# Performance work log

Hardware: AMD Instinct MI355X
Metric: run time of the kernel (lower is better)

Reference implementation:

```python
import jax, jax.numpy as jnp
import numpy as np

N = 4096          # samples per domain
D_IN = 512        # input feature dim
H = 10            # hidden size of featurizer
D_OUT = 50        # featurizer output dim


def setup_inputs() -> dict:
    key = jax.random.key(0)
    ks = jax.random.split(key, 12)
    def lin(k, fan_in, fan_out):
        bound = 1.0 / np.sqrt(fan_in)
        kw, kb = jax.random.split(k)
        W = jax.random.uniform(kw, (fan_in, fan_out), jnp.float32, -bound, bound)
        b = jax.random.uniform(kb, (fan_out,), jnp.float32, -bound, bound)
        return W, b
    W1, b1 = lin(ks[0], D_IN, H)
    W2, b2 = lin(ks[1], H, H)
    W3, b3 = lin(ks[2], H, H)
    W4, b4 = lin(ks[3], H, D_OUT)
    Xs = jax.random.normal(ks[4], (N, D_IN), jnp.float32)
    Xt = jax.random.normal(ks[5], (N, D_IN), jnp.float32) + 0.1
    # epsilonOPT = log(rand(1) * 1e-10)
    epsilonOPT = jnp.log(jax.random.uniform(ks[6], (1,), jnp.float32) * 1e-10)
    sigmaOPT = jnp.sqrt(jnp.asarray(2.0 * 32 * 32, jnp.float32))
    sigma0OPT = jnp.sqrt(jnp.asarray(0.005, jnp.float32))
    return {"Xs": Xs, "Xt": Xt, "W1": W1, "b1": b1, "W2": W2, "b2": b2,
            "W3": W3, "b3": b3, "W4": W4, "b4": b4,
            "epsilonOPT": epsilonOPT, "sigmaOPT": sigmaOPT, "sigma0OPT": sigma0OPT}


def _pdist2(x, y):
    # squared pairwise distances, clamped at 0 (as in Pdist2)
    xn = jnp.sum(x * x, axis=1)[:, None]
    yn = jnp.sum(y * y, axis=1)[None, :]
    d = xn + yn - 2.0 * (x @ y.T)
    return jnp.maximum(d, 0.0)


def _featurize(x, W1, b1, W2, b2, W3, b3, W4, b4):
    sp = jax.nn.softplus
    h = sp(x @ W1 + b1)
    h = sp(h @ W2 + b2)
    h = sp(h @ W3 + b3)
    return h @ W4 + b4


def _deep_kernel(Dd, Do, ep, sigma, sigma0):
    # (1-ep)*exp(-Dd/sigma0 - Do/sigma) + ep*exp(-Do/sigma)   (L=1)
    e_org = jnp.exp(-Do / sigma)
    return (1.0 - ep) * jnp.exp(-Dd / sigma0) * e_org + ep * e_org


def reference(Xs, Xt, W1, b1, W2, b2, W3, b3, W4, b4, epsilonOPT, sigmaOPT, sigma0OPT):
    n = Xs.shape[0]
    Fea_org = jnp.concatenate([Xs, Xt], axis=0)
    Fea = _featurize(Fea_org, W1, b1, W2, b2, W3, b3, W4, b4)

    ep = jax.nn.sigmoid(epsilonOPT)[0]
    sigma = sigmaOPT ** 2
    sigma0 = sigma0OPT ** 2

    X, Y = Fea[:n], Fea[n:]
    Xo, Yo = Fea_org[:n], Fea_org[n:]

    Kx = _deep_kernel(_pdist2(X, X), _pdist2(Xo, Xo), ep, sigma, sigma0)
    Ky = _deep_kernel(_pdist2(Y, Y), _pdist2(Yo, Yo), ep, sigma, sigma0)
    Kxy = _deep_kernel(_pdist2(X, Y), _pdist2(Xo, Yo), ep, sigma, sigma0)

    nx = n
    ny = Fea.shape[0] - n
    # unbiased estimator with use_1sample_U=True
    xx = (jnp.sum(Kx) - jnp.trace(Kx)) / (nx * (nx - 1))
    yy = (jnp.sum(Ky) - jnp.trace(Ky)) / (ny * (ny - 1))
    xy = (jnp.sum(Kxy) - jnp.trace(Kxy)) / (nx * (ny - 1))
    mmd2 = xx - 2.0 * xy + yy
    return mmd2
```

## Files before the change

### kernel.cpp

```cpp
#include <hip/hip_runtime.h>
#include <math.h>

#define NHALF 4096
#define NTOT  8192
#define DIN   512
#define DFR   50
#define FPS   160
#define BM    128
#define NBI   64
#define NTRI  2080
#define T64STRIDE 524288
#define KCSTRIDE  65536

typedef short short8 __attribute__((ext_vector_type(8)));
typedef float f32x4 __attribute__((ext_vector_type(4)));
typedef int   i32x8 __attribute__((ext_vector_type(8)));

__device__ __forceinline__ float softplus_f(float x) {
    return fmaxf(x, 0.f) + log1pf(expf(-fabsf(x)));
}

__device__ __forceinline__ unsigned cvt_pk_bf16(float lo, float hi) {
    unsigned r;
    asm("v_cvt_pk_bf16_f32 %0, %1, %2" : "=v"(r) : "v"(lo), "v"(hi));
    return r;
}

__device__ __forceinline__ unsigned short bf16_rne(float v) {
    return (unsigned short)(cvt_pk_bf16(v, 0.f) & 0xffffu);
}

__device__ __forceinline__ float bf16_to_f(unsigned short s) {
    union { unsigned u; float f; } c;
    c.u = (unsigned)s << 16;
    return c.f;
}

__device__ __forceinline__ void gload_lds16(const void* g, void* l) {
    __builtin_amdgcn_global_load_lds(
        (const __attribute__((address_space(1))) void*)g,
        (__attribute__((address_space(3))) void*)l, 16, 0, 0);
}

__global__ __launch_bounds__(256) void featurize_kernel(
    const float* __restrict__ Xs, const float* __restrict__ Xt,
    const float* __restrict__ W1, const float* __restrict__ b1,
    const float* __restrict__ W2, const float* __restrict__ b2,
    const float* __restrict__ W3, const float* __restrict__ b3,
    const float* __restrict__ W4, const float* __restrict__ b4,
    const float* __restrict__ sigP, const float* __restrict__ sig0P,
    unsigned short* __restrict__ FpkA, unsigned short* __restrict__ FpkB,
    float* __restrict__ normC, char* __restrict__ Xb8)
{
    __shared__ float W1L[80 * 65];
    __shared__ __align__(16) unsigned short pkA[4][FPS];
    __shared__ __align__(16) unsigned short pkB[4][FPS];
    int tid = threadIdx.x;
    for (int e = tid; e < 5120; e += 256) {
        int r = e / 10, j = e - 10 * r;
        W1L[((r & 7) * 10 + j) * 65 + (r >> 3)] = W1[e];
    }
    __syncthreads();

    int row  = (blockIdx.x * blockDim.x + tid) >> 6;
    int lane = tid & 63, wv = tid >> 6;
    float alpha8 = 64.f / sigP[0];
    float beta   = 64.f / sig0P[0];
    const float* src = (row < NHALF) ? (Xs + (size_t)row * DIN)
                                     : (Xt + (size_t)(row - NHALF) * DIN);
    float4 v0 = ((const float4*)src)[lane * 2];
    float4 v1 = ((const float4*)src)[lane * 2 + 1];
    float x[8] = {v0.x, v0.y, v0.z, v0.w, v1.x, v1.y, v1.z, v1.w};

    float z[8];
#pragma unroll
    for (int t = 0; t < 8; ++t) z[t] = x[t] * alpha8;
    unsigned w0 = 0, w1 = 0;
    w0 = __builtin_amdgcn_cvt_pk_fp8_f32(z[0], z[1], w0, false);
    w0 = __builtin_amdgcn_cvt_pk_fp8_f32(z[2], z[3], w0, true);
    w1 = __builtin_amdgcn_cvt_pk_fp8_f32(z[4], z[5], w1, false);
    w1 = __builtin_amdgcn_cvt_pk_fp8_f32(z[6], z[7], w1, true);
    float on = 0.f, qf;
    qf = __builtin_amdgcn_cvt_f32_fp8(w0, 0); on = fmaf(qf, qf, on);
    qf = __builtin_amdgcn_cvt_f32_fp8(w0, 1); on = fmaf(qf, qf, on);
    qf = __builtin_amdgcn_cvt_f32_fp8(w0, 2); on = fmaf(qf, qf, on);
    qf = __builtin_amdgcn_cvt_f32_fp8(w0, 3); on = fmaf(qf, qf, on);
    qf = __builtin_amdgcn_cvt_f32_fp8(w1, 0); on = fmaf(qf, qf, on);
    qf = __builtin_amdgcn_cvt_f32_fp8(w1, 1); on = fmaf(qf, qf, on);
    qf = __builtin_amdgcn_cvt_f32_fp8(w1, 2); on = fmaf(qf, qf, on);
    qf = __builtin_amdgcn_cvt_f32_fp8(w1, 3); on = fmaf(qf, qf, on);
    *(uint2*)(Xb8 + (lane >> 3) * T64STRIDE + (lane & 7) * KCSTRIDE
              + (size_t)row * 8) = make_uint2(w0, w1);

    float p[10];
#pragma unroll
    for (int j = 0; j < 10; ++j) p[j] = 0.f;
#pragma unroll
    for (int t = 0; t < 8; ++t) {
        float xv = x[t];
#pragma unroll
        for (int j = 0; j < 10; ++j)
            p[j] = fmaf(xv, W1L[(t * 10 + j) * 65 + lane], p[j]);
    }
#pragma unroll
    for (int m = 32; m >= 1; m >>= 1) {
#pragma unroll
        for (int j = 0; j < 10; ++j) p[j] += __shfl_xor(p[j], m, 64);
        on += __shfl_xor(on, m, 64);
    }
    int lane10 = lane % 10;
    float pown = p[0];
#pragma unroll
    for (int j = 1; j < 10; ++j) pown = (lane10 == j) ? p[j] : pown;
    float hown = softplus_f(pown + b1[lane10]);
    float h1b[10];
#pragma unroll
    for (int k = 0; k < 10; ++k) h1b[k] = __shfl(hown, k, 64);

    float a2 = b2[lane10];
#pragma unroll
    for (int k = 0; k < 10; ++k) a2 = fmaf(h1b[k], W2[k * 10 + lane10], a2);
    float h2own = softplus_f(a2);
    float h2b[10];
#pragma unroll
    for (int k = 0; k < 10; ++k) h2b[k] = __shfl(h2own, k, 64);

    float a3 = b3[lane10];
#pragma unroll
    for (int k = 0; k < 10; ++k) a3 = fmaf(h2b[k], W3[k * 10 + lane10], a3);
    float h3own = softplus_f(a3);
    float h3b[10];
#pragma unroll
    for (int k = 0; k < 10; ++k) h3b[k] = __shfl(h3own, k, 64);

    float o = 0.f;
    if (lane < DFR) {
        float a = b4[lane];
#pragma unroll
        for (int k = 0; k < 10; ++k) a = fmaf(h3b[k], W4[k * 50 + lane], a);
        o = a;
    }
    float f = o * beta;
    unsigned short hi_s = bf16_rne(f);
    unsigned short lo_s = bf16_rne(f - bf16_to_f(hi_s));
    if (lane < DFR) {
        pkA[wv][lane] = hi_s;  pkA[wv][50 + lane] = hi_s;  pkA[wv][100 + lane] = lo_s;
        pkB[wv][lane] = hi_s;  pkB[wv][50 + lane] = lo_s;  pkB[wv][100 + lane] = hi_s;
    } else if (lane < 60) {
        pkA[wv][100 + lane] = 0;
        pkB[wv][100 + lane] = 0;
    }
    __syncthreads();
    if (lane < 20)
        *(uint4*)(FpkA + (size_t)row * FPS + lane * 8) = *(const uint4*)&pkA[wv][lane * 8];
    else if (lane < 40)
        *(uint4*)(FpkB + (size_t)row * FPS + (lane - 20) * 8) = *(const uint4*)&pkB[wv][(lane - 20) * 8];

    float fn = f * f;
#pragma unroll
    for (int m = 32; m >= 1; m >>= 1) fn += __shfl_xor(fn, m, 64);
    if (lane == 0) normC[row] = (on + fn) * (1.f / 4096.f);
}

__global__ __launch_bounds__(256, 3) void pairwise_kernel(
    const char* __restrict__ Xb8,
    const unsigned short* __restrict__ FpkA,
    const unsigned short* __restrict__ FpkB,
    const float* __restrict__ normC,
    double* __restrict__ partialsC)
{
    __shared__ char smem[49152] __attribute__((aligned(128)));
    __shared__ double sredC[4];

    int bid = blockIdx.x;
    int bi = (int)((129.0 - sqrt(16641.0 - 8.0 * (double)bid)) * 0.5);
    while (NBI * (bi + 1) - (bi + 1) * bi / 2 <= bid) ++bi;
    while (NBI * bi - bi * (bi - 1) / 2 > bid) --bi;
    int bj = bi + (bid - (NBI * bi - bi * (bi - 1) / 2));

    int tid = threadIdx.x;
    int lane = tid & 63, wave = tid >> 6;
    int g = lane >> 4, l15 = lane & 15;
    int i0w = (wave >> 1) * 64;
    int j0w = (wave & 1) * 64;
    int ri = bi * BM, rj = bj * BM;

    const char* sA8 = Xb8 + wave * KCSTRIDE + (size_t)(ri + 2 * lane) * 8;
    const char* sB8 = Xb8 + wave * KCSTRIDE + (size_t)(rj + 2 * lane) * 8;
    int srow = tid >> 2;
    int schunk = (tid & 3) ^ ((srow >> 1) & 3);
    const char* fA0 = (const char*)(FpkA + (size_t)(ri + srow) * FPS) + schunk * 16;
    const char* fB0 = (const char*)(FpkB + (size_t)(rj + srow) * FPS) + schunk * 16;
    char* lwave = (char*)smem + wave * 1024;

    int swz = (l15 >> 1) & 3;
    int offA = (i0w + l15) * 32 + (g ^ swz) * 8;
    int offB = (j0w + l15) * 32 + (g ^ swz) * 8;

    f32x4 acc[4][4];
#pragma unroll
    for (int a = 0; a < 4; ++a)
#pragma unroll
        for (int b = 0; b < 4; ++b) acc[a][b] = (f32x4){0.f, 0.f, 0.f, 0.f};

#define STAGE8(kt, buf)                                              \
    do {                                                             \
        char* ld_ = lwave + (buf) * 16384;                           \
        const char* a_ = sA8 + (kt) * T64STRIDE;                     \
        const char* b_ = sB8 + (kt) * T64STRIDE;                     \
        gload_lds16(a_,                ld_);                         \
        gload_lds16(a_ + 4 * KCSTRIDE, ld_ + 4096);                  \
        gload_lds16(b_,                ld_ + 8192);                  \
        gload_lds16(b_ + 4 * KCSTRIDE, ld_ + 12288);                 \
    } while (0)

#define STAGEF(kf, buf)                                              \
    do {                                                             \
        char* ld_ = lwave + (buf) * 16384;                           \
        const char* gA_ = fA0 + (kf) * 64;                           \
        const char* gB_ = fB0 + (kf) * 64;                           \
        gload_lds16(gA_,         ld_);                               \
        gload_lds16(gA_ + 20480, ld_ + 4096);                        \
        gload_lds16(gB_,         ld_ + 8192);                        \
        gload_lds16(gB_ + 20480, ld_ + 12288);                       \
    } while (0)

#define C128(pa, pb)                                                               \
    do {                                                                           \
        const char* slA_ = smem + (((lane & 32) ? (pb) : (pa)) * 16384);           \
        int kcb_ = ((lane >> 4) & 1) << 2;                                         \
        const char* baseA_ = slA_ + kcb_ * 1024 + (i0w + l15) * 8;                 \
        const char* baseB_ = slA_ + 8192 + kcb_ * 1024 + (j0w + l15) * 8;          \
        i32x8 af_[4];                                                              \
        _Pragma("unroll")                                                          \
        for (int a = 0; a < 4; ++a) {                                              \
            const char* p_ = baseA_ + a * 128;                                     \
            uint2 t0 = *(const uint2*)(p_);                                        \
            uint2 t1 = *(const uint2*)(p_ + 1024);                                 \
            uint2 t2 = *(const uint2*)(p_ + 2048);                                 \
            uint2 t3 = *(const uint2*)(p_ + 3072);                                 \
            af_[a] = (i32x8){(int)t0.x, (int)t0.y, (int)t1.x, (int)t1.y,           \
                             (int)t2.x, (int)t2.y, (int)t3.x, (int)t3.y};          \
        }                                                                          \
        __builtin_amdgcn_s_setprio(1);                                             \
        _Pragma("unroll")                                                          \
        for (int b = 0; b < 4; ++b) {                                              \
            const char* p_ = baseB_ + b * 128;                                     \
            uint2 t0 = *(const uint2*)(p_);                                        \
            uint2 t1 = *(const uint2*)(p_ + 1024);                                 \
            uint2 t2 = *(const uint2*)(p_ + 2048);                                 \
            uint2 t3 = *(const uint2*)(p_ + 3072);                                 \
            i32x8 bf_ = (i32x8){(int)t0.x, (int)t0.y, (int)t1.x, (int)t1.y,        \
                                (int)t2.x, (int)t2.y, (int)t3.x, (int)t3.y};       \
            _Pragma("unroll")                                                      \
            for (int a = 0; a < 4; ++a)                                            \
                acc[a][b] = __builtin_amdgcn_mfma_scale_f32_16x16x128_f8f6f4(      \
                    af_[a], bf_, acc[a][b], 0, 0,                                  \
                    0, 0x7f7f7f7f, 0, 0x7f7f7f7f);                                 \
        }                                                                          \
        __builtin_amdgcn_s_setprio(0);                                             \
    } while (0)

#define C16(buf)                                                                   \
    do {                                                                           \
        const unsigned short* tc_ = (const unsigned short*)(smem + (buf) * 16384); \
        short8 af_[4], bf_[4];                                                     \
        _Pragma("unroll")                                                          \
        for (int a = 0; a < 4; ++a)                                                \
            af_[a] = *(const short8*)(tc_ + offA + a * 512);                       \
        _Pragma("unroll")                                                          \
        for (int b = 0; b < 4; ++b)                                                \
            bf_[b] = *(const short8*)(tc_ + 4096 + offB + b * 512);                \
        __builtin_amdgcn_s_setprio(1);                                             \
        _Pragma("unroll")                                                          \
        for (int a = 0; a < 4; ++a)                                                \
            _Pragma("unroll")                                                      \
            for (int b = 0; b < 4; ++b)                                            \
                acc[a][b] = __builtin_amdgcn_mfma_f32_16x16x32_bf16(               \
                    af_[a], bf_[b], acc[a][b], 0, 0, 0);                           \
        __builtin_amdgcn_s_setprio(0);                                             \
    } while (0)

#define WAITV(N) do { asm volatile("s_waitcnt vmcnt(" #N ")" ::: "memory");        \
                      __builtin_amdgcn_sched_barrier(0); } while (0)
#define BARR1    do { __builtin_amdgcn_s_barrier();                                \
                      __builtin_amdgcn_sched_barrier(0); } while (0)
#define BARR2    do { __builtin_amdgcn_sched_barrier(0);                           \
                      asm volatile("s_waitcnt lgkmcnt(0)" ::: "memory");           \
                      __builtin_amdgcn_sched_barrier(0);                           \
                      __builtin_amdgcn_s_barrier();                                \
                      __builtin_amdgcn_sched_barrier(0); } while (0)

    STAGE8(0, 0); STAGE8(1, 1); STAGE8(2, 2);
    WAITV(4); BARR1; C128(0, 1); BARR2; STAGE8(3, 0); STAGE8(4, 1);
    WAITV(4); BARR1; C128(2, 0); BARR2; STAGE8(5, 2); STAGE8(6, 0);
    WAITV(4); BARR1; C128(1, 2); BARR2; STAGE8(7, 1); STAGEF(0, 2);
    WAITV(4); BARR1; C128(0, 1); BARR2; STAGEF(1, 0); STAGEF(2, 1);
    WAITV(8); BARR1; C16(2); BARR2; STAGEF(3, 2);
    WAITV(8); BARR1; C16(0); BARR2; STAGEF(4, 0);
    WAITV(8); BARR1; C16(1);
    WAITV(4); BARR1; C16(2);
    WAITV(0); BARR1; C16(0);

    float nci[16], ncj[4];
#pragma unroll
    for (int a = 0; a < 4; ++a)
#pragma unroll
        for (int r = 0; r < 4; ++r)
            nci[a * 4 + r] = normC[ri + i0w + 16 * a + 4 * g + r];
#pragma unroll
    for (int b = 0; b < 4; ++b)
        ncj[b] = normC[rj + j0w + 16 * b + l15];

    float sgn = ((ri < NHALF) == (rj < NHALF)) ? 1.f : -1.f;
    float wsgn = 2.f * sgn;
    const float cf = 2.f / 4096.f;

    float locf = 0.f;
#pragma unroll
    for (int a = 0; a < 4; ++a)
#pragma unroll
        for (int b = 0; b < 4; ++b)
#pragma unroll
            for (int r = 0; r < 4; ++r) {
                int gi = ri + i0w + 16 * a + 4 * g + r;
                int gj = rj + j0w + 16 * b + l15;
                float Dc = fmaxf(fmaf(-cf, acc[a][b][r], nci[a * 4 + r] + ncj[b]), 0.f);
                float K = __expf(-Dc);
                float w = (gj > gi && gj != gi + NHALF) ? wsgn : 0.f;
                locf = fmaf(w, K, locf);
            }
    double loc = (double)locf;
#pragma unroll
    for (int m = 32; m >= 1; m >>= 1) loc += __shfl_xor(loc, m, 64);
    if (lane == 0) sredC[wave] = loc;
    __syncthreads();
    if (tid == 0)
        partialsC[bid] = sredC[0] + sredC[1] + sredC[2] + sredC[3];
#undef STAGE8
#undef STAGEF
#undef C128
#undef C16
#undef WAITV
#undef BARR1
#undef BARR2
}

__global__ __launch_bounds__(256) void reduce_kernel(
    const double* __restrict__ partialsC, float* __restrict__ out)
{
    double s = 0.0;
    for (int i = threadIdx.x; i < NTRI; i += 256) s += partialsC[i];
#pragma unroll
    for (int m = 32; m >= 1; m >>= 1) s += __shfl_xor(s, m, 64);
    __shared__ double ss[4];
    int w = threadIdx.x >> 6;
    if ((threadIdx.x & 63) == 0) ss[w] = s;
    __syncthreads();
    if (threadIdx.x == 0) {
        double S = ss[0] + ss[1] + ss[2] + ss[3];
        out[0] = (float)(S / (4096.0 * 4095.0));
    }
}

extern "C" void kernel_launch(void* const* d_in, const int* in_sizes, int n_in,
                              void* d_out, int out_size, void* d_ws, size_t ws_size,
                              hipStream_t stream)
{
    const float* Xs  = (const float*)d_in[0];
    const float* Xt  = (const float*)d_in[1];
    const float* W1  = (const float*)d_in[2];
    const float* b1  = (const float*)d_in[3];
    const float* W2  = (const float*)d_in[4];
    const float* b2  = (const float*)d_in[5];
    const float* W3  = (const float*)d_in[6];
    const float* b3  = (const float*)d_in[7];
    const float* W4  = (const float*)d_in[8];
    const float* b4  = (const float*)d_in[9];
    const float* sigP  = (const float*)d_in[11];
    const float* sig0P = (const float*)d_in[12];
    float* out = (float*)d_out;

    char* ws = (char*)d_ws;
    char* Xb8 = ws;
    unsigned short* FpkA = (unsigned short*)(ws + 8 * T64STRIDE);
    unsigned short* FpkB = FpkA + (size_t)NTOT * FPS;
    float* normC = (float*)(FpkB + (size_t)NTOT * FPS);
    double* partialsC = (double*)(normC + NTOT);

    featurize_kernel<<<dim3(2048), dim3(256), 0, stream>>>(
        Xs, Xt, W1, b1, W2, b2, W3, b3, W4, b4, sigP, sig0P,
        FpkA, FpkB, normC, Xb8);
    pairwise_kernel<<<dim3(NTRI), dim3(256), 0, stream>>>(
        Xb8, FpkA, FpkB, normC, partialsC);
    reduce_kernel<<<dim3(1), dim3(256), 0, stream>>>(partialsC, out);
}
```

Measured before the change: 65.43 us.

## Fuse final reduction into pairwise kernel via fixed-point atomics; halve featurize grid

```diff
diff --git a/kernel.cpp b/kernel.cpp
--- a/kernel.cpp
+++ b/kernel.cpp
@@ -11,6 +11,7 @@
 #define NTRI  2080
 #define T64STRIDE 524288
 #define KCSTRIDE  65536
+#define FIXSCALE  16777216.0
 
 typedef short short8 __attribute__((ext_vector_type(8)));
 typedef float f32x4 __attribute__((ext_vector_type(4)));
@@ -62,104 +63,106 @@
     }
     __syncthreads();
 
-    int row  = (blockIdx.x * blockDim.x + tid) >> 6;
     int lane = tid & 63, wv = tid >> 6;
+    int lane10 = lane % 10;
     float alpha8 = 64.f / sigP[0];
     float beta   = 64.f / sig0P[0];
-    const float* src = (row < NHALF) ? (Xs + (size_t)row * DIN)
-                                     : (Xt + (size_t)(row - NHALF) * DIN);
-    float4 v0 = ((const float4*)src)[lane * 2];
-    float4 v1 = ((const float4*)src)[lane * 2 + 1];
-    float x[8] = {v0.x, v0.y, v0.z, v0.w, v1.x, v1.y, v1.z, v1.w};
-
-    float z[8];
-#pragma unroll
-    for (int t = 0; t < 8; ++t) z[t] = x[t] * alpha8;
-    unsigned w0 = 0, w1 = 0;
-    w0 = __builtin_amdgcn_cvt_pk_fp8_f32(z[0], z[1], w0, false);
-    w0 = __builtin_amdgcn_cvt_pk_fp8_f32(z[2], z[3], w0, true);
-    w1 = __builtin_amdgcn_cvt_pk_fp8_f32(z[4], z[5], w1, false);
-    w1 = __builtin_amdgcn_cvt_pk_fp8_f32(z[6], z[7], w1, true);
-    float on = 0.f, qf;
-    qf = __builtin_amdgcn_cvt_f32_fp8(w0, 0); on = fmaf(qf, qf, on);
-    qf = __builtin_amdgcn_cvt_f32_fp8(w0, 1); on = fmaf(qf, qf, on);
-    qf = __builtin_amdgcn_cvt_f32_fp8(w0, 2); on = fmaf(qf, qf, on);
-    qf = __builtin_amdgcn_cvt_f32_fp8(w0, 3); on = fmaf(qf, qf, on);
-    qf = __builtin_amdgcn_cvt_f32_fp8(w1, 0); on = fmaf(qf, qf, on);
-    qf = __builtin_amdgcn_cvt_f32_fp8(w1, 1); on = fmaf(qf, qf, on);
-    qf = __builtin_amdgcn_cvt_f32_fp8(w1, 2); on = fmaf(qf, qf, on);
-    qf = __builtin_amdgcn_cvt_f32_fp8(w1, 3); on = fmaf(qf, qf, on);
-    *(uint2*)(Xb8 + (lane >> 3) * T64STRIDE + (lane & 7) * KCSTRIDE
-              + (size_t)row * 8) = make_uint2(w0, w1);
-
-    float p[10];
-#pragma unroll
-    for (int j = 0; j < 10; ++j) p[j] = 0.f;
-#pragma unroll
-    for (int t = 0; t < 8; ++t) {
-        float xv = x[t];
-#pragma unroll
-        for (int j = 0; j < 10; ++j)
-            p[j] = fmaf(xv, W1L[(t * 10 + j) * 65 + lane], p[j]);
+
+    for (int it = 0; it < 2; ++it) {
+        int row = blockIdx.x * 8 + wv * 2 + it;
+        const float* src = (row < NHALF) ? (Xs + (size_t)row * DIN)
+                                         : (Xt + (size_t)(row - NHALF) * DIN);
+        float4 v0 = ((const float4*)src)[lane * 2];
+        float4 v1 = ((const float4*)src)[lane * 2 + 1];
+        float x[8] = {v0.x, v0.y, v0.z, v0.w, v1.x, v1.y, v1.z, v1.w};
+
+        float z[8];
+#pragma unroll
+        for (int t = 0; t < 8; ++t) z[t] = x[t] * alpha8;
+        unsigned w0 = 0, w1 = 0;
+        w0 = __builtin_amdgcn_cvt_pk_fp8_f32(z[0], z[1], w0, false);
+        w0 = __builtin_amdgcn_cvt_pk_fp8_f32(z[2], z[3], w0, true);
+        w1 = __builtin_amdgcn_cvt_pk_fp8_f32(z[4], z[5], w1, false);
+        w1 = __builtin_amdgcn_cvt_pk_fp8_f32(z[6], z[7], w1, true);
+        float on = 0.f, qf;
+        qf = __builtin_amdgcn_cvt_f32_fp8(w0, 0); on = fmaf(qf, qf, on);
+        qf = __builtin_amdgcn_cvt_f32_fp8(w0, 1); on = fmaf(qf, qf, on);
+        qf = __builtin_amdgcn_cvt_f32_fp8(w0, 2); on = fmaf(qf, qf, on);
+        qf = __builtin_amdgcn_cvt_f32_fp8(w0, 3); on = fmaf(qf, qf, on);
+        qf = __builtin_amdgcn_cvt_f32_fp8(w1, 0); on = fmaf(qf, qf, on);
+        qf = __builtin_amdgcn_cvt_f32_fp8(w1, 1); on = fmaf(qf, qf, on);
+        qf = __builtin_amdgcn_cvt_f32_fp8(w1, 2); on = fmaf(qf, qf, on);
+        qf = __builtin_amdgcn_cvt_f32_fp8(w1, 3); on = fmaf(qf, qf, on);
+        *(uint2*)(Xb8 + (lane >> 3) * T64STRIDE + (lane & 7) * KCSTRIDE
+                  + (size_t)row * 8) = make_uint2(w0, w1);
+
+        float p[10];
+#pragma unroll
+        for (int j = 0; j < 10; ++j) p[j] = 0.f;
+#pragma unroll
+        for (int t = 0; t < 8; ++t) {
+            float xv = x[t];
+#pragma unroll
+            for (int j = 0; j < 10; ++j)
+                p[j] = fmaf(xv, W1L[(t * 10 + j) * 65 + lane], p[j]);
+        }
+#pragma unroll
+        for (int m = 32; m >= 1; m >>= 1) {
+#pragma unroll
+            for (int j = 0; j < 10; ++j) p[j] += __shfl_xor(p[j], m, 64);
+            on += __shfl_xor(on, m, 64);
+        }
+        float pown = p[0];
+#pragma unroll
+        for (int j = 1; j < 10; ++j) pown = (lane10 == j) ? p[j] : pown;
+        float hown = softplus_f(pown + b1[lane10]);
+        float h1b[10];
+#pragma unroll
+        for (int k = 0; k < 10; ++k) h1b[k] = __shfl(hown, k, 64);
+
+        float a2 = b2[lane10];
+#pragma unroll
+        for (int k = 0; k < 10; ++k) a2 = fmaf(h1b[k], W2[k * 10 + lane10], a2);
+        float h2own = softplus_f(a2);
+        float h2b[10];
+#pragma unroll
+        for (int k = 0; k < 10; ++k) h2b[k] = __shfl(h2own, k, 64);
+
+        float a3 = b3[lane10];
+#pragma unroll
+        for (int k = 0; k < 10; ++k) a3 = fmaf(h2b[k], W3[k * 10 + lane10], a3);
+        float h3own = softplus_f(a3);
+        float h3b[10];
+#pragma unroll
+        for (int k = 0; k < 10; ++k) h3b[k] = __shfl(h3own, k, 64);
+
+        float o = 0.f;
+        if (lane < DFR) {
+            float a = b4[lane];
+#pragma unroll
+            for (int k = 0; k < 10; ++k) a = fmaf(h3b[k], W4[k * 50 + lane], a);
+            o = a;
+        }
+        float f = o * beta;
+        unsigned short hi_s = bf16_rne(f);
+        unsigned short lo_s = bf16_rne(f - bf16_to_f(hi_s));
+        if (lane < DFR) {
+            pkA[wv][lane] = hi_s;  pkA[wv][50 + lane] = hi_s;  pkA[wv][100 + lane] = lo_s;
+            pkB[wv][lane] = hi_s;  pkB[wv][50 + lane] = lo_s;  pkB[wv][100 + lane] = hi_s;
+        } else if (lane < 60) {
+            pkA[wv][100 + lane] = 0;
+            pkB[wv][100 + lane] = 0;
+        }
+        if (lane < 20)
+            *(uint4*)(FpkA + (size_t)row * FPS + lane * 8) = *(const uint4*)&pkA[wv][lane * 8];
+        else if (lane < 40)
+            *(uint4*)(FpkB + (size_t)row * FPS + (lane - 20) * 8) = *(const uint4*)&pkB[wv][(lane - 20) * 8];
+
+        float fn = f * f;
+#pragma unroll
+        for (int m = 32; m >= 1; m >>= 1) fn += __shfl_xor(fn, m, 64);
+        if (lane == 0) normC[row] = (on + fn) * (1.f / 4096.f);
     }
-#pragma unroll
-    for (int m = 32; m >= 1; m >>= 1) {
-#pragma unroll
-        for (int j = 0; j < 10; ++j) p[j] += __shfl_xor(p[j], m, 64);
-        on += __shfl_xor(on, m, 64);
-    }
-    int lane10 = lane % 10;
-    float pown = p[0];
-#pragma unroll
-    for (int j = 1; j < 10; ++j) pown = (lane10 == j) ? p[j] : pown;
-    float hown = softplus_f(pown + b1[lane10]);
-    float h1b[10];
-#pragma unroll
-    for (int k = 0; k < 10; ++k) h1b[k] = __shfl(hown, k, 64);
-
-    float a2 = b2[lane10];
-#pragma unroll
-    for (int k = 0; k < 10; ++k) a2 = fmaf(h1b[k], W2[k * 10 + lane10], a2);
-    float h2own = softplus_f(a2);
-    float h2b[10];
-#pragma unroll
-    for (int k = 0; k < 10; ++k) h2b[k] = __shfl(h2own, k, 64);
-
-    float a3 = b3[lane10];
-#pragma unroll
-    for (int k = 0; k < 10; ++k) a3 = fmaf(h2b[k], W3[k * 10 + lane10], a3);
-    float h3own = softplus_f(a3);
-    float h3b[10];
-#pragma unroll
-    for (int k = 0; k < 10; ++k) h3b[k] = __shfl(h3own, k, 64);
-
-    float o = 0.f;
-    if (lane < DFR) {
-        float a = b4[lane];
-#pragma unroll
-        for (int k = 0; k < 10; ++k) a = fmaf(h3b[k], W4[k * 50 + lane], a);
-        o = a;
-    }
-    float f = o * beta;
-    unsigned short hi_s = bf16_rne(f);
-    unsigned short lo_s = bf16_rne(f - bf16_to_f(hi_s));
-    if (lane < DFR) {
-        pkA[wv][lane] = hi_s;  pkA[wv][50 + lane] = hi_s;  pkA[wv][100 + lane] = lo_s;
-        pkB[wv][lane] = hi_s;  pkB[wv][50 + lane] = lo_s;  pkB[wv][100 + lane] = hi_s;
-    } else if (lane < 60) {
-        pkA[wv][100 + lane] = 0;
-        pkB[wv][100 + lane] = 0;
-    }
-    __syncthreads();
-    if (lane < 20)
-        *(uint4*)(FpkA + (size_t)row * FPS + lane * 8) = *(const uint4*)&pkA[wv][lane * 8];
-    else if (lane < 40)
-        *(uint4*)(FpkB + (size_t)row * FPS + (lane - 20) * 8) = *(const uint4*)&pkB[wv][(lane - 20) * 8];
-
-    float fn = f * f;
-#pragma unroll
-    for (int m = 32; m >= 1; m >>= 1) fn += __shfl_xor(fn, m, 64);
-    if (lane == 0) normC[row] = (on + fn) * (1.f / 4096.f);
 }
 
 __global__ __launch_bounds__(256, 3) void pairwise_kernel(
@@ -167,7 +170,9 @@
     const unsigned short* __restrict__ FpkA,
     const unsigned short* __restrict__ FpkB,
     const float* __restrict__ normC,
-    double* __restrict__ partialsC)
+    unsigned long long* __restrict__ accI,
+    unsigned int* __restrict__ doneCnt,
+    float* __restrict__ out)
 {
     __shared__ char smem[49152] __attribute__((aligned(128)));
     __shared__ double sredC[4];
@@ -335,8 +340,19 @@
     for (int m = 32; m >= 1; m >>= 1) loc += __shfl_xor(loc, m, 64);
     if (lane == 0) sredC[wave] = loc;
     __syncthreads();
-    if (tid == 0)
-        partialsC[bid] = sredC[0] + sredC[1] + sredC[2] + sredC[3];
+    if (tid == 0) {
+        double S = sredC[0] + sredC[1] + sredC[2] + sredC[3];
+        long long q = (long long)llrint(S * FIXSCALE);
+        atomicAdd(accI, (unsigned long long)q);
+        __threadfence();
+        unsigned done = atomicAdd(doneCnt, 1u);
+        if (done == NTRI - 1) {
+            __threadfence();
+            unsigned long long raw = atomicAdd(accI, 0ULL);
+            double tot = (double)(long long)raw / FIXSCALE;
+            out[0] = (float)(tot / (4096.0 * 4095.0));
+        }
+    }
 #undef STAGE8
 #undef STAGEF
 #undef C128
@@ -344,23 +360,6 @@
 #undef WAITV
 #undef BARR1
 #undef BARR2
-}
-
-__global__ __launch_bounds__(256) void reduce_kernel(
-    const double* __restrict__ partialsC, float* __restrict__ out)
-{
-    double s = 0.0;
-    for (int i = threadIdx.x; i < NTRI; i += 256) s += partialsC[i];
-#pragma unroll
-    for (int m = 32; m >= 1; m >>= 1) s += __shfl_xor(s, m, 64);
-    __shared__ double ss[4];
-    int w = threadIdx.x >> 6;
-    if ((threadIdx.x & 63) == 0) ss[w] = s;
-    __syncthreads();
-    if (threadIdx.x == 0) {
-        double S = ss[0] + ss[1] + ss[2] + ss[3];
-        out[0] = (float)(S / (4096.0 * 4095.0));
-    }
 }
 
 extern "C" void kernel_launch(void* const* d_in, const int* in_sizes, int n_in,
@@ -386,12 +385,14 @@
     unsigned short* FpkA = (unsigned short*)(ws + 8 * T64STRIDE);
     unsigned short* FpkB = FpkA + (size_t)NTOT * FPS;
     float* normC = (float*)(FpkB + (size_t)NTOT * FPS);
-    double* partialsC = (double*)(normC + NTOT);
-
-    featurize_kernel<<<dim3(2048), dim3(256), 0, stream>>>(
+    unsigned long long* accI = (unsigned long long*)(normC + NTOT);
+    unsigned int* doneCnt = (unsigned int*)(accI + 1);
+
+    hipMemsetAsync((void*)accI, 0, 16, stream);
+
+    featurize_kernel<<<dim3(1024), dim3(256), 0, stream>>>(
         Xs, Xt, W1, b1, W2, b2, W3, b3, W4, b4, sigP, sig0P,
         FpkA, FpkB, normC, Xb8);
     pairwise_kernel<<<dim3(NTRI), dim3(256), 0, stream>>>(
-        Xb8, FpkA, FpkB, normC, partialsC);
-    reduce_kernel<<<dim3(1), dim3(256), 0, stream>>>(partialsC, out);
-}
+        Xb8, FpkA, FpkB, normC, accI, doneCnt, out);
+}
```

New measurement: 119.8 us. +83.1%, slower.
